# Kernel optimization log

Hardware: AMD Instinct MI355X
Metric: run time of the kernel (lower is better)

The kernel has to match this reference:

```python
import jax, jax.numpy as jnp
import numpy as np

N, E = 50000, 800000
HID, EDGE_DIM, HEADS = 128, 16, 4
C = HID // HEADS  # 32
NEG_SLOPE = 0.2  # GATv2Conv default negative_slope


def setup_inputs() -> dict:
    key = jax.random.key(0)
    ks = jax.random.split(key, 16)
    def glorot(k, shape):
        fan_in = shape[0]
        return jax.random.normal(k, shape, jnp.float32) / np.sqrt(fan_in)
    return {
        "x": jax.random.normal(ks[0], (N, HID), jnp.float32),
        "edge_index": jax.random.randint(ks[1], (2, E), 0, N, jnp.int64 if jax.config.jax_enable_x64 else jnp.int32),
        "edge_attr": jax.random.normal(ks[2], (E, EDGE_DIM), jnp.float32),
        # GATv2Conv params (lin_l, lin_r with bias; lin_edge bias-free; att; final bias)
        "Wl": glorot(ks[3], (HID, HID)),
        "bl": jnp.zeros((HID,), jnp.float32),
        "Wr": glorot(ks[4], (HID, HID)),
        "br": jnp.zeros((HID,), jnp.float32),
        "We": glorot(ks[5], (EDGE_DIM, HID)),
        "att": glorot(ks[6], (HEADS, C)),
        "bias_gat": jnp.zeros((HID,), jnp.float32),
        # RMSNorm weights
        "w_norm1": jnp.ones((HID,), jnp.float32),
        "w_norm2": jnp.ones((HID,), jnp.float32),
        # FFN params
        "ffn_w1": glorot(ks[7], (HID, 4 * HID)),
        "ffn_b1": jnp.zeros((4 * HID,), jnp.float32),
        "ffn_w2": glorot(ks[8], (4 * HID, HID)),
        "ffn_b2": jnp.zeros((HID,), jnp.float32),
    }


def rmsnorm(x, w):
    # torch.nn.RMSNorm with eps=None -> eps = finfo(dtype).eps
    eps = jnp.finfo(x.dtype).eps
    ms = jnp.mean(x * x, axis=-1, keepdims=True)
    return x * jax.lax.rsqrt(ms + eps) * w


def gatv2_conv(x, edge_index, edge_attr, Wl, bl, Wr, br, We, att, bias_gat):
    n = x.shape[0]
    h, c = att.shape
    xl = (x @ Wl + bl).reshape(n, h, c)   # source-side transform (x_j)
    xr = (x @ Wr + br).reshape(n, h, c)   # target-side transform (x_i)
    src, dst = edge_index[0], edge_index[1]
    e = (edge_attr @ We).reshape(-1, h, c)
    m = xl[src] + xr[dst] + e                       # [E, H, C] per-edge message pre-activation
    s = jnp.where(m > 0, m, NEG_SLOPE * m)          # LeakyReLU(0.2)
    logits = jnp.einsum('ehc,hc->eh', s, att)       # [E, H]
    # scatter-softmax over edges grouped by target node
    lmax = jax.ops.segment_max(logits, dst, num_segments=n)
    ex = jnp.exp(logits - lmax[dst])
    den = jax.ops.segment_sum(ex, dst, num_segments=n)
    alpha = ex / (den[dst] + 1e-16)                 # PyG softmax denominator guard
    out = jax.ops.segment_sum(alpha[..., None] * xl[src], dst, num_segments=n)
    return out.reshape(n, h * c) + bias_gat


def reference(x, edge_index, edge_attr, Wl, bl, Wr, br, We, att, bias_gat,
              w_norm1, w_norm2, ffn_w1, ffn_b1, ffn_w2, ffn_b2):
    x_attn = gatv2_conv(x, edge_index, edge_attr, Wl, bl, Wr, br, We, att, bias_gat)
    h = rmsnorm(x + x_attn, w_norm1)
    f = jax.nn.gelu(h @ ffn_w1 + ffn_b1, approximate=False) @ ffn_w2 + ffn_b2
    return rmsnorm(h + f, w_norm2)
```

## Files before the change

kernel.cpp:

```cpp
#include <hip/hip_runtime.h>

#define NN 50000
#define EE 800000

typedef unsigned short u16;

#define OFF_GAT  0u
#define OFF_XLB  6400000u
#define OFF_XRB  9600000u
#define OFF_SE   12800000u
#define OFF_CNT  14400000u
#define OFF_OFS  14450000u
#define OFF_H    6400000u
#define OFF_HB   12800000u
#define OFF_WLRT 16000000u
#define OFF_W1T  16016384u
#define OFF_W2T  16049152u

#define RMS_EPS 1.1920928955078125e-7f

typedef float f32x4v __attribute__((ext_vector_type(4)));
typedef short s16x8 __attribute__((ext_vector_type(8)));

__device__ __forceinline__ f32x4v mfma16(s16x8 a, s16x8 b, f32x4v c) {
  return __builtin_amdgcn_mfma_f32_16x16x32_bf16(a, b, c, 0, 0, 0);
}
__device__ __forceinline__ u16 f2b(float f) {
  unsigned int u = __float_as_uint(f);
  unsigned int r = (u + 0x7fffu + ((u >> 16) & 1u)) >> 16;
  return (u16)r;
}
__device__ __forceinline__ float b2f(u16 u) {
  union { float f; unsigned int i; } x; x.i = ((unsigned int)u) << 16; return x.f;
}
__device__ __forceinline__ s16x8 ld_bf16x8_f32(const float* __restrict__ p) {
  float4 v0 = *(const float4*)p;
  float4 v1 = *(const float4*)(p + 4);
  s16x8 r;
  r[0] = (short)f2b(v0.x); r[1] = (short)f2b(v0.y);
  r[2] = (short)f2b(v0.z); r[3] = (short)f2b(v0.w);
  r[4] = (short)f2b(v1.x); r[5] = (short)f2b(v1.y);
  r[6] = (short)f2b(v1.z); r[7] = (short)f2b(v1.w);
  return r;
}
__device__ __forceinline__ int readlane_i32(int v, int lane) {
  return __builtin_amdgcn_readlane(v, lane);
}
__device__ __forceinline__ float gelu_fast(float x) {
  float x2 = x * x;
  float y = x * fmaf(0.07135481283f, x2, 1.5957691216f);
  float e = __expf(-y);
  return x * __builtin_amdgcn_rcpf(1.0f + e);
}

__global__ __launch_bounds__(256) void k_prep(const float* __restrict__ Wl, const float* __restrict__ Wr,
    const float* __restrict__ W1, const float* __restrict__ W2,
    int* __restrict__ cnt, u16* __restrict__ wlrt, u16* __restrict__ w1t, u16* __restrict__ w2t)
{
  int i = blockIdx.x * 256 + threadIdx.x;
  if (i < NN) cnt[i] = 0;
  if (i < 32768) {
    int n = i >> 7, k = i & 127;
    float v = (n < 128) ? Wl[k * 128 + n] : Wr[k * 128 + (n - 128)];
    wlrt[i] = f2b(v);
  }
  {
    int n = i >> 7, k = i & 127;
    w1t[i] = f2b(W1[k * 512 + n]);
  }
  {
    int n = i >> 9, k = i & 511;
    w2t[i] = f2b(W2[k * 128 + n]);
  }
}

__global__ __launch_bounds__(256) void k_hist(const int* __restrict__ ei, int* __restrict__ cnt) {
  int e = blockIdx.x * 256 + threadIdx.x;
  if (e < EE) atomicAdd(&cnt[ei[EE + e]], 1);
}

__global__ __launch_bounds__(1024) void k_scan(const int* __restrict__ cnt,
    int* __restrict__ offs, int* __restrict__ pos)
{
  __shared__ int wsum[16];
  __shared__ int carry_s;
  int tid = threadIdx.x, lane = tid & 63, wv = tid >> 6;
  if (tid == 0) carry_s = 0;
  __syncthreads();
  for (int base = 0; base < NN; base += 1024) {
    int i = base + tid;
    int v = (i < NN) ? cnt[i] : 0;
    int x = v;
#pragma unroll
    for (int ofs = 1; ofs < 64; ofs <<= 1) {
      int y = __shfl_up(x, ofs);
      if (lane >= ofs) x += y;
    }
    if (lane == 63) wsum[wv] = x;
    __syncthreads();
    if (wv == 0) {
      int s = (lane < 16) ? wsum[lane] : 0;
#pragma unroll
      for (int ofs = 1; ofs < 16; ofs <<= 1) {
        int y = __shfl_up(s, ofs);
        if (lane >= ofs) s += y;
      }
      if (lane < 16) wsum[lane] = s;
    }
    __syncthreads();
    int wbase = (wv > 0) ? wsum[wv - 1] : 0;
    int incl = x + wbase + carry_s;
    if (i < NN) { offs[i + 1] = incl; pos[i] = incl - v; }
    if (base == 0 && tid == 0) offs[0] = 0;
    __syncthreads();
    if (tid == 1023) carry_s = incl;
    __syncthreads();
  }
}

__global__ __launch_bounds__(256) void k_permute(const int* __restrict__ ei,
    int* __restrict__ pos, int2* __restrict__ se)
{
  int e = blockIdx.x * 256 + threadIdx.x;
  if (e < EE) {
    int slot = atomicAdd(&pos[ei[EE + e]], 1);
    se[slot] = make_int2(ei[e], e);
  }
}

__global__ __launch_bounds__(256) void k1_mfma(const float* __restrict__ x, const u16* __restrict__ wlrt,
    const float* __restrict__ bl, const float* __restrict__ br,
    u16* __restrict__ xlb, u16* __restrict__ xrb)
{
  int tid = threadIdx.x;
  int w = tid >> 6, lane = tid & 63;
  int quad = lane >> 4, l16 = lane & 15;
  int row0 = blockIdx.x * 32;
  int ko = quad * 8;
  f32x4v acc[2][4];
#pragma unroll
  for (int mt = 0; mt < 2; ++mt)
#pragma unroll
    for (int nt = 0; nt < 4; ++nt) acc[mt][nt] = (f32x4v){0.f, 0.f, 0.f, 0.f};
#pragma unroll
  for (int ks = 0; ks < 4; ++ks) {
    int k0 = ks * 32 + ko;
    s16x8 a[2];
#pragma unroll
    for (int mt = 0; mt < 2; ++mt) {
      int row = row0 + mt * 16 + l16; if (row >= NN) row = NN - 1;
      a[mt] = ld_bf16x8_f32(x + row * 128 + k0);
    }
#pragma unroll
    for (int nt = 0; nt < 4; ++nt) {
      int col = w * 64 + nt * 16 + l16;
      s16x8 b = *(const s16x8*)(wlrt + col * 128 + k0);
      acc[0][nt] = mfma16(a[0], b, acc[0][nt]);
      acc[1][nt] = mfma16(a[1], b, acc[1][nt]);
    }
  }
#pragma unroll
  for (int nt = 0; nt < 4; ++nt) {
    int col = w * 64 + nt * 16 + l16;
    bool isl = col < 128;
    float bias = isl ? bl[col] : br[col - 128];
    u16* dst = isl ? xlb : xrb;
    int cc = isl ? col : col - 128;
#pragma unroll
    for (int mt = 0; mt < 2; ++mt)
#pragma unroll
      for (int r = 0; r < 4; ++r) {
        int row = row0 + mt * 16 + quad * 4 + r;
        if (row < NN) dst[row * 128 + cc] = f2b(acc[mt][nt][r] + bias);
      }
  }
}

__global__ __launch_bounds__(256) void k2_attn(
    const int* __restrict__ offs, const int2* __restrict__ se,
    const float* __restrict__ eattr,
    const float* __restrict__ att, const float* __restrict__ We,
    const u16* __restrict__ xlb, const u16* __restrict__ xrb,
    float* __restrict__ gat)
{
  __shared__ float epbuf[4][16 * 128];
  int l = threadIdx.x & 63;
  int wv = threadIdx.x >> 6;
  int l16 = l & 15, quad = l >> 4;
  int wid = (blockIdx.x * blockDim.x + threadIdx.x) >> 6;
  int nw = (gridDim.x * blockDim.x) >> 6;
  int c0 = 2 * l;
  float* epl = epbuf[wv];

  s16x8 bfrag[8];
  {
    bool kz = quad >= 2;
    int kb = (quad & 1) * 8;
#pragma unroll
    for (int t = 0; t < 8; ++t) {
      s16x8 b;
#pragma unroll
      for (int e = 0; e < 8; ++e) {
        float v = kz ? 0.f : We[(kb + e) * 128 + t * 16 + l16];
        b[e] = (short)f2b(v);
      }
      bfrag[t] = b;
    }
  }
  float a0 = att[c0], a1 = att[c0 + 1];

  for (int d = wid; d < NN; d += nw) {
    int start = offs[d];
    int deg = offs[d + 1] - start;
    ushort2 xru = *(const ushort2*)(xrb + d * 128 + c0);
    float xr0 = b2f(xru.x), xr1 = b2f(xru.y);
    float mh = -1e30f, lh = 0.f, O0 = 0.f, O1 = 0.f;
    for (int base = 0; base < deg; base += 64) {
      bool act = (base + l) < deg;
      int idx = start + base + l;
      int2 sev = act ? se[idx] : make_int2(0, 0);
      int cnt = min(64, deg - base);
      for (int sub16 = 0; sub16 < cnt; sub16 += 16) {
        int eidv = __shfl(sev.y, sub16 + l16);
        s16x8 afrag = ld_bf16x8_f32(eattr + (size_t)eidv * 16 + (quad & 1) * 8);
#pragma unroll
        for (int t = 0; t < 8; ++t) {
          f32x4v ac = mfma16(afrag, bfrag[t], (f32x4v){0.f, 0.f, 0.f, 0.f});
          int cb = t * 16 + l16;
#pragma unroll
          for (int r = 0; r < 4; ++r)
            epl[(quad * 4 + r) * 128 + cb] = ac[r];
        }
        int cend = min(sub16 + 16, cnt);
        for (int sub = sub16; sub < cend; sub += 4) {
          float p[4], xl0v[4], xl1v[4];
#pragma unroll
          for (int j2 = 0; j2 < 4; ++j2) {
            int sr = readlane_i32(sev.x, sub + j2);
            float2 epv = *(const float2*)&epl[(sub - sub16 + j2) * 128 + c0];
            ushort2 xlu = *(const ushort2*)(xlb + (size_t)sr * 128 + c0);
            float xl0 = b2f(xlu.x), xl1 = b2f(xlu.y);
            float m0 = xl0 + xr0 + epv.x;
            float m1 = xl1 + xr1 + epv.y;
            float s0 = m0 > 0.f ? m0 : 0.2f * m0;
            float s1 = m1 > 0.f ? m1 : 0.2f * m1;
            p[j2] = fmaf(s0, a0, s1 * a1);
            xl0v[j2] = xl0; xl1v[j2] = xl1;
          }
#pragma unroll
          for (int o = 1; o <= 8; o <<= 1) {
            p[0] += __shfl_xor(p[0], o);
            p[1] += __shfl_xor(p[1], o);
            p[2] += __shfl_xor(p[2], o);
            p[3] += __shfl_xor(p[3], o);
          }
#pragma unroll
          for (int j2 = 0; j2 < 4; ++j2) if (sub + j2 >= cnt) p[j2] = -1e30f;
          float nm = fmaxf(fmaxf(fmaxf(p[0], p[1]), fmaxf(p[2], p[3])), mh);
          float sc = __expf(mh - nm);
          float w0 = __expf(p[0] - nm), w1 = __expf(p[1] - nm);
          float w2 = __expf(p[2] - nm), w3 = __expf(p[3] - nm);
          lh = fmaf(lh, sc, (w0 + w1) + (w2 + w3));
          O0 = fmaf(O0, sc, fmaf(w0, xl0v[0], fmaf(w1, xl0v[1], fmaf(w2, xl0v[2], w3 * xl0v[3]))));
          O1 = fmaf(O1, sc, fmaf(w0, xl1v[0], fmaf(w1, xl1v[1], fmaf(w2, xl1v[2], w3 * xl1v[3]))));
          mh = nm;
        }
      }
    }
    float inv = 1.f / (lh + 1e-16f);
    *(float2*)(gat + d * 128 + c0) = make_float2(O0 * inv, O1 * inv);
  }
}

__global__ __launch_bounds__(256) void k5_norm1(const float* __restrict__ x,
    const float* __restrict__ gat, const float* __restrict__ bg,
    const float* __restrict__ wn1, float* __restrict__ h, u16* __restrict__ hb)
{
  int l = threadIdx.x & 63;
  int row = blockIdx.x * 4 + (threadIdx.x >> 6);
  int c0 = 2 * l;
  float2 xu = *(const float2*)(x + row * 128 + c0);
  float2 gv = *(const float2*)(gat + row * 128 + c0);
  float2 bu = *(const float2*)(bg + c0);
  float v0 = xu.x + gv.x + bu.x;
  float v1 = xu.y + gv.y + bu.y;
  float ss = v0 * v0 + v1 * v1;
#pragma unroll
  for (int o = 1; o < 64; o <<= 1) ss += __shfl_xor(ss, o);
  float rr = rsqrtf(ss * (1.f / 128.f) + RMS_EPS);
  float2 wu = *(const float2*)(wn1 + c0);
  float o0 = v0 * rr * wu.x, o1 = v1 * rr * wu.y;
  *(float2*)(h + row * 128 + c0) = make_float2(o0, o1);
  ushort2 hu; hu.x = f2b(o0); hu.y = f2b(o1);
  *(ushort2*)(hb + row * 128 + c0) = hu;
}

__device__ __forceinline__ u16* tls_addr(u16* tls, int row, int col) {
  int byte = (row << 10) + (col << 1);
  byte ^= (row & 7) << 4;
  return (u16*)((char*)tls + byte);
}

__global__ __launch_bounds__(512) void k6_mfma(const float* __restrict__ h,
    const u16* __restrict__ hb,
    const u16* __restrict__ w1t, const u16* __restrict__ w2t,
    const float* __restrict__ b1, const float* __restrict__ b2,
    const float* __restrict__ wn2, float* __restrict__ out)
{
  __shared__ u16 tls[32 * 512];
  int tid = threadIdx.x;
  int w = tid >> 6, lane = tid & 63;
  int quad = lane >> 4, l16 = lane & 15;
  int row0 = blockIdx.x * 32;
  int ko = quad * 8;

  f32x4v acc1[2][4];
#pragma unroll
  for (int mt = 0; mt < 2; ++mt)
#pragma unroll
    for (int nt = 0; nt < 4; ++nt) acc1[mt][nt] = (f32x4v){0.f, 0.f, 0.f, 0.f};
#pragma unroll
  for (int ks = 0; ks < 4; ++ks) {
    int k0 = ks * 32 + ko;
    s16x8 a[2];
#pragma unroll
    for (int mt = 0; mt < 2; ++mt) {
      int row = row0 + mt * 16 + l16; if (row >= NN) row = NN - 1;
      a[mt] = *(const s16x8*)(hb + row * 128 + k0);
    }
#pragma unroll
    for (int nt = 0; nt < 4; ++nt) {
      int col = w * 64 + nt * 16 + l16;
      s16x8 b = *(const s16x8*)(w1t + col * 128 + k0);
      acc1[0][nt] = mfma16(a[0], b, acc1[0][nt]);
      acc1[1][nt] = mfma16(a[1], b, acc1[1][nt]);
    }
  }
#pragma unroll
  for (int nt = 0; nt < 4; ++nt) {
    int col = w * 64 + nt * 16 + l16;
    float bb = b1[col];
#pragma unroll
    for (int mt = 0; mt < 2; ++mt)
#pragma unroll
      for (int r = 0; r < 4; ++r) {
        float t = gelu_fast(acc1[mt][nt][r] + bb);
        *tls_addr(tls, mt * 16 + quad * 4 + r, col) = f2b(t);
      }
  }
  __syncthreads();

  f32x4v acc2[2];
  acc2[0] = (f32x4v){0.f, 0.f, 0.f, 0.f};
  acc2[1] = (f32x4v){0.f, 0.f, 0.f, 0.f};
  int col = w * 16 + l16;
  const u16* bptr = w2t + col * 512;
#pragma unroll
  for (int ks = 0; ks < 16; ++ks) {
    int k0 = ks * 32 + ko;
    s16x8 a2[2];
#pragma unroll
    for (int mt = 0; mt < 2; ++mt)
      a2[mt] = *(const s16x8*)tls_addr(tls, mt * 16 + l16, k0);
    s16x8 b = *(const s16x8*)(bptr + k0);
    acc2[0] = mfma16(a2[0], b, acc2[0]);
    acc2[1] = mfma16(a2[1], b, acc2[1]);
  }

  float bb2 = b2[col], wn = wn2[col];
  float ov[2][4];
#pragma unroll
  for (int mt = 0; mt < 2; ++mt)
#pragma unroll
    for (int r = 0; r < 4; ++r) {
      int row = row0 + mt * 16 + quad * 4 + r;
      int rowc = row < NN ? row : NN - 1;
      ov[mt][r] = h[rowc * 128 + col] + acc2[mt][r] + bb2;
    }
  __syncthreads();
  float (*red)[32] = (float (*)[32])(void*)tls;
#pragma unroll
  for (int mt = 0; mt < 2; ++mt)
#pragma unroll
    for (int r = 0; r < 4; ++r) {
      float q = ov[mt][r] * ov[mt][r];
      q += __shfl_xor(q, 1); q += __shfl_xor(q, 2);
      q += __shfl_xor(q, 4); q += __shfl_xor(q, 8);
      if (l16 == 0) red[w][mt * 16 + quad * 4 + r] = q;
    }
  __syncthreads();
#pragma unroll
  for (int mt = 0; mt < 2; ++mt)
#pragma unroll
    for (int r = 0; r < 4; ++r) {
      int rl = mt * 16 + quad * 4 + r;
      float tot = ((red[0][rl] + red[1][rl]) + (red[2][rl] + red[3][rl]))
                + ((red[4][rl] + red[5][rl]) + (red[6][rl] + red[7][rl]));
      float rr = rsqrtf(tot * (1.f / 128.f) + RMS_EPS);
      int row = row0 + rl;
      if (row < NN) out[row * 128 + col] = ov[mt][r] * rr * wn;
    }
}

extern "C" void kernel_launch(void* const* d_in, const int* in_sizes, int n_in,
                              void* d_out, int out_size, void* d_ws, size_t ws_size,
                              hipStream_t stream) {
  const float* x   = (const float*)d_in[0];
  const int*   ei  = (const int*)d_in[1];
  const float* ea  = (const float*)d_in[2];
  const float* Wl  = (const float*)d_in[3];
  const float* bl  = (const float*)d_in[4];
  const float* Wr  = (const float*)d_in[5];
  const float* br  = (const float*)d_in[6];
  const float* We  = (const float*)d_in[7];
  const float* att = (const float*)d_in[8];
  const float* bg  = (const float*)d_in[9];
  const float* wn1 = (const float*)d_in[10];
  const float* wn2 = (const float*)d_in[11];
  const float* W1  = (const float*)d_in[12];
  const float* b1  = (const float*)d_in[13];
  const float* W2  = (const float*)d_in[14];
  const float* b2  = (const float*)d_in[15];

  float* wsf = (float*)d_ws;
  int*   wsi = (int*)d_ws;

  float* gat  = wsf + OFF_GAT;
  u16* xlb    = (u16*)(wsf + OFF_XLB);
  u16* xrb    = (u16*)(wsf + OFF_XRB);
  int2* se    = (int2*)(wsf + OFF_SE);
  int* cnt    = wsi + OFF_CNT;
  int* pos    = wsi + OFF_CNT;
  int* offs   = wsi + OFF_OFS;
  float* hbuf = wsf + OFF_H;
  u16* hb     = (u16*)(wsf + OFF_HB);
  u16* wlrt   = (u16*)(wsf + OFF_WLRT);
  u16* w1t    = (u16*)(wsf + OFF_W1T);
  u16* w2t    = (u16*)(wsf + OFF_W2T);

  k_prep<<<256, 256, 0, stream>>>(Wl, Wr, W1, W2, cnt, wlrt, w1t, w2t);

  k_hist<<<(EE + 255) / 256, 256, 0, stream>>>(ei, cnt);
  k_scan<<<1, 1024, 0, stream>>>(cnt, offs, pos);
  k_permute<<<(EE + 255) / 256, 256, 0, stream>>>(ei, pos, se);

  k1_mfma<<<(NN + 31) / 32, 256, 0, stream>>>(x, wlrt, bl, br, xlb, xrb);

  k2_attn<<<1024, 256, 0, stream>>>(offs, se, ea, att, We, xlb, xrb, gat);

  k5_norm1<<<NN / 4, 256, 0, stream>>>(x, gat, bg, wn1, hbuf, hb);

  k6_mfma<<<(NN + 31) / 32, 512, 0, stream>>>(hbuf, hb, w1t, w2t, b1, b2, wn2, (float*)d_out);
}
```

Baseline: 536.4 us.

## Restructure GATv2 attention to keep edge projections in registers via transposed MFMA

The attention kernel now swaps the MFMA operands so each lane holds the edge-feature projection for its own edge (lanes map to edges, quads to channel slices), which removes the LDS staging buffer and its store/load round trip. Logits for 16 edges are computed in parallel, with a cross-quad shuffle tree per head and one online-softmax update per 16-edge chunk instead of per 4 edges. The weighted sum over xl is then accumulated in a serial per-edge loop that gathers xl rows again. The grid is also doubled. The cost is higher register pressure from the per-lane xr/xl/ep arrays and a second gather of xl.

```diff
diff --git a/kernel.cpp b/kernel.cpp
--- a/kernel.cpp
+++ b/kernel.cpp
@@ -183,87 +183,110 @@
     const u16* __restrict__ xlb, const u16* __restrict__ xrb,
     float* __restrict__ gat)
 {
-  __shared__ float epbuf[4][16 * 128];
   int l = threadIdx.x & 63;
-  int wv = threadIdx.x >> 6;
   int l16 = l & 15, quad = l >> 4;
   int wid = (blockIdx.x * blockDim.x + threadIdx.x) >> 6;
   int nw = (gridDim.x * blockDim.x) >> 6;
   int c0 = 2 * l;
-  float* epl = epbuf[wv];
-
-  s16x8 bfrag[8];
-  {
-    bool kz = quad >= 2;
-    int kb = (quad & 1) * 8;
-#pragma unroll
-    for (int t = 0; t < 8; ++t) {
-      s16x8 b;
-#pragma unroll
-      for (int e = 0; e < 8; ++e) {
-        float v = kz ? 0.f : We[(kb + e) * 128 + t * 16 + l16];
-        b[e] = (short)f2b(v);
-      }
-      bfrag[t] = b;
-    }
-  }
-  float a0 = att[c0], a1 = att[c0 + 1];
+  bool kz = quad >= 2;
+  int kb = (quad & 1) * 8;
+
+  s16x8 wfrag[8];
+#pragma unroll
+  for (int t = 0; t < 8; ++t) {
+    s16x8 b;
+#pragma unroll
+    for (int e = 0; e < 8; ++e) {
+      float v = kz ? 0.f : We[(kb + e) * 128 + t * 16 + l16];
+      b[e] = (short)f2b(v);
+    }
+    wfrag[t] = b;
+  }
+  float4 attf[8];
+#pragma unroll
+  for (int t = 0; t < 8; ++t) attf[t] = *(const float4*)(att + t * 16 + quad * 4);
 
   for (int d = wid; d < NN; d += nw) {
     int start = offs[d];
     int deg = offs[d + 1] - start;
-    ushort2 xru = *(const ushort2*)(xrb + d * 128 + c0);
-    float xr0 = b2f(xru.x), xr1 = b2f(xru.y);
+    ushort4 xr_u[8];
+#pragma unroll
+    for (int t = 0; t < 8; ++t)
+      xr_u[t] = *(const ushort4*)(xrb + d * 128 + t * 16 + quad * 4);
     float mh = -1e30f, lh = 0.f, O0 = 0.f, O1 = 0.f;
+
     for (int base = 0; base < deg; base += 64) {
       bool act = (base + l) < deg;
       int idx = start + base + l;
       int2 sev = act ? se[idx] : make_int2(0, 0);
       int cnt = min(64, deg - base);
       for (int sub16 = 0; sub16 < cnt; sub16 += 16) {
-        int eidv = __shfl(sev.y, sub16 + l16);
-        s16x8 afrag = ld_bf16x8_f32(eattr + (size_t)eidv * 16 + (quad & 1) * 8);
+        int vcnt = min(16, cnt - sub16);
+        int eid_b = __shfl(sev.y, sub16 + l16);
+        int src_b = __shfl(sev.x, sub16 + l16);
+
+        s16x8 eaf = ld_bf16x8_f32(eattr + (size_t)eid_b * 16 + kb);
+
+        f32x4v ep[8];
+#pragma unroll
+        for (int t = 0; t < 8; ++t)
+          ep[t] = mfma16(wfrag[t], eaf, (f32x4v){0.f, 0.f, 0.f, 0.f});
+
+        ushort4 xl_u[8];
+#pragma unroll
+        for (int t = 0; t < 8; ++t)
+          xl_u[t] = *(const ushort4*)(xlb + (size_t)src_b * 128 + t * 16 + quad * 4);
+
+        float ph[4] = {0.f, 0.f, 0.f, 0.f};
 #pragma unroll
         for (int t = 0; t < 8; ++t) {
-          f32x4v ac = mfma16(afrag, bfrag[t], (f32x4v){0.f, 0.f, 0.f, 0.f});
-          int cb = t * 16 + l16;
-#pragma unroll
-          for (int r = 0; r < 4; ++r)
-            epl[(quad * 4 + r) * 128 + cb] = ac[r];
+          int h = t >> 1;
+          float4 av = attf[t];
+          float m0 = ep[t][0] + b2f(xr_u[t].x) + b2f(xl_u[t].x);
+          float m1 = ep[t][1] + b2f(xr_u[t].y) + b2f(xl_u[t].y);
+          float m2 = ep[t][2] + b2f(xr_u[t].z) + b2f(xl_u[t].z);
+          float m3 = ep[t][3] + b2f(xr_u[t].w) + b2f(xl_u[t].w);
+          float s0 = fmaxf(m0, 0.2f * m0);
+          float s1 = fmaxf(m1, 0.2f * m1);
+          float s2 = fmaxf(m2, 0.2f * m2);
+          float s3 = fmaxf(m3, 0.2f * m3);
+          ph[h] = fmaf(s0, av.x, ph[h]);
+          ph[h] = fmaf(s1, av.y, ph[h]);
+          ph[h] = fmaf(s2, av.z, ph[h]);
+          ph[h] = fmaf(s3, av.w, ph[h]);
         }
-        int cend = min(sub16 + 16, cnt);
-        for (int sub = sub16; sub < cend; sub += 4) {
-          float p[4], xl0v[4], xl1v[4];
-#pragma unroll
-          for (int j2 = 0; j2 < 4; ++j2) {
-            int sr = readlane_i32(sev.x, sub + j2);
-            float2 epv = *(const float2*)&epl[(sub - sub16 + j2) * 128 + c0];
-            ushort2 xlu = *(const ushort2*)(xlb + (size_t)sr * 128 + c0);
-            float xl0 = b2f(xlu.x), xl1 = b2f(xlu.y);
-            float m0 = xl0 + xr0 + epv.x;
-            float m1 = xl1 + xr1 + epv.y;
-            float s0 = m0 > 0.f ? m0 : 0.2f * m0;
-            float s1 = m1 > 0.f ? m1 : 0.2f * m1;
-            p[j2] = fmaf(s0, a0, s1 * a1);
-            xl0v[j2] = xl0; xl1v[j2] = xl1;
-          }
-#pragma unroll
-          for (int o = 1; o <= 8; o <<= 1) {
-            p[0] += __shfl_xor(p[0], o);
-            p[1] += __shfl_xor(p[1], o);
-            p[2] += __shfl_xor(p[2], o);
-            p[3] += __shfl_xor(p[3], o);
-          }
-#pragma unroll
-          for (int j2 = 0; j2 < 4; ++j2) if (sub + j2 >= cnt) p[j2] = -1e30f;
-          float nm = fmaxf(fmaxf(fmaxf(p[0], p[1]), fmaxf(p[2], p[3])), mh);
-          float sc = __expf(mh - nm);
-          float w0 = __expf(p[0] - nm), w1 = __expf(p[1] - nm);
-          float w2 = __expf(p[2] - nm), w3 = __expf(p[3] - nm);
-          lh = fmaf(lh, sc, (w0 + w1) + (w2 + w3));
-          O0 = fmaf(O0, sc, fmaf(w0, xl0v[0], fmaf(w1, xl0v[1], fmaf(w2, xl0v[2], w3 * xl0v[3]))));
-          O1 = fmaf(O1, sc, fmaf(w0, xl1v[0], fmaf(w1, xl1v[1], fmaf(w2, xl1v[2], w3 * xl1v[3]))));
-          mh = nm;
+        bool q0 = (quad & 1) != 0, q1 = (quad & 2) != 0;
+        float S0 = q0 ? ph[0] : ph[1];
+        float S1 = q0 ? ph[2] : ph[3];
+        float R0 = __shfl_xor(S0, 16);
+        float R1 = __shfl_xor(S1, 16);
+        float Q0 = (q0 ? ph[1] : ph[0]) + R0;
+        float Q1 = (q0 ? ph[3] : ph[2]) + R1;
+        float S2 = q1 ? Q0 : Q1;
+        float R2 = __shfl_xor(S2, 32);
+        float lg = (q1 ? Q1 : Q0) + R2;
+        if (l16 >= vcnt) lg = -1e30f;
+
+        float bm = lg;
+#pragma unroll
+        for (int o = 1; o <= 8; o <<= 1) bm = fmaxf(bm, __shfl_xor(bm, o));
+        float nm = fmaxf(mh, bm);
+        float sc = __expf(mh - nm);
+        float w = __expf(lg - nm);
+        float bs = w;
+#pragma unroll
+        for (int o = 1; o <= 8; o <<= 1) bs += __shfl_xor(bs, o);
+        lh = fmaf(lh, sc, bs);
+        O0 *= sc; O1 *= sc;
+        mh = nm;
+
+        int lbase = l & 48;
+        for (int e = 0; e < vcnt; ++e) {
+          float we = __shfl(w, lbase + e);
+          int sr = readlane_i32(sev.x, sub16 + e);
+          ushort2 xlu = *(const ushort2*)(xlb + (size_t)sr * 128 + c0);
+          O0 = fmaf(we, b2f(xlu.x), O0);
+          O1 = fmaf(we, b2f(xlu.y), O1);
         }
       }
     }
@@ -398,7 +421,9 @@
                 + ((red[4][rl] + red[5][rl]) + (red[6][rl] + red[7][rl]));
       float rr = rsqrtf(tot * (1.f / 128.f) + RMS_EPS);
       int row = row0 + rl;
-      if (row < NN) out[row * 128 + col] = ov[mt][r] * rr * wn;
+      if (row < NN) {
+        out[row * 128 + col] = ov[mt][r] * rr * wn;
+      }
     }
 }
 
@@ -446,7 +471,7 @@
 
   k1_mfma<<<(NN + 31) / 32, 256, 0, stream>>>(x, wlrt, bl, br, xlb, xrb);
 
-  k2_attn<<<1024, 256, 0, stream>>>(offs, se, ea, att, We, xlb, xrb, gat);
+  k2_attn<<<2048, 256, 0, stream>>>(offs, se, ea, att, We, xlb, xrb, gat);
 
   k5_norm1<<<NN / 4, 256, 0, stream>>>(x, gat, bg, wn1, hbuf, hb);
 
```

Result: slower. 620.7 us (+15.7%).
